# Optimization experiments

Hardware: AMD Instinct MI355X
Metric: run time of the kernel (lower is better)

## Reference

```python
import jax, jax.numpy as jnp
import numpy as np

B, N, F_IN = 32, 512, 64
HEADS = (8, 8)
HIDS = (64, 64)
EDGE_P = 0.05  # graph density
NEG_SLOPE = 0.2
NEG_INF = -1e20


def setup_inputs() -> dict:
    key = jax.random.key(0)
    ks = jax.random.split(key, 8)
    x = jax.random.normal(ks[0], (B, N, F_IN), dtype=jnp.float32)
    adj = (jax.random.uniform(ks[1], (B, N, N)) < EDGE_P).astype(jnp.float32)
    adj = jnp.maximum(adj, adj.transpose(0, 2, 1))  # symmetric adjacency
    # mask = (batch, row): every (b, n) pair gets the masked softmax
    b_idx = jnp.repeat(jnp.arange(B, dtype=jnp.int32), N)   # [B*N]
    r_idx = jnp.tile(jnp.arange(N, dtype=jnp.int32), B)     # [B*N]
    # layer 0: f_in=64 -> f_out=64, H=8 ; layer 1: f_in=64*8=512 -> f_out=64, H=8
    W0 = jax.random.normal(ks[2], (F_IN, HIDS[0]), dtype=jnp.float32) / jnp.sqrt(jnp.float32(F_IN))
    a_src0 = jax.random.normal(ks[3], (HIDS[0], HEADS[0]), dtype=jnp.float32) / jnp.sqrt(jnp.float32(HIDS[0]))
    a_dst0 = jax.random.normal(ks[4], (HIDS[0], HEADS[0]), dtype=jnp.float32) / jnp.sqrt(jnp.float32(HIDS[0]))
    f_in1 = HIDS[0] * HEADS[0]
    W1 = jax.random.normal(ks[5], (f_in1, HIDS[1]), dtype=jnp.float32) / jnp.sqrt(jnp.float32(f_in1))
    a_src1 = jax.random.normal(ks[6], (HIDS[1], HEADS[1]), dtype=jnp.float32) / jnp.sqrt(jnp.float32(HIDS[1]))
    a_dst1 = jax.random.normal(ks[7], (HIDS[1], HEADS[1]), dtype=jnp.float32) / jnp.sqrt(jnp.float32(HIDS[1]))
    return dict(x=x, adj=adj, b_idx=b_idx, r_idx=r_idx,
                W0=W0, a_src0=a_src0, a_dst0=a_dst0,
                W1=W1, a_src1=a_src1, a_dst1=a_dst1)


def _gat_layer(x, adj, b_idx, r_idx, W, a_src, a_dst):
    # x: [B,N,f_in], adj: [B,N,N] (diag already set), W: [f_in,F], a_*: [F,H]
    hp = x @ W                                        # [B,N,F]
    s = jnp.einsum('bnf,fh->bhn', hp, a_src)          # attn_src
    d = jnp.einsum('bnf,fh->bhn', hp, a_dst)          # attn_dst
    attn = s[:, :, :, None] + d[:, :, None, :]        # [B,H,N,N]
    attn = jnp.where(attn >= 0, attn, NEG_SLOPE * attn)  # leaky_relu(0.2)
    attn = jnp.where(adj[:, None, :, :] == 0, 0.0, attn)  # masked_fill(adj==0, 0)
    rows = attn[b_idx, :, r_idx, :]                   # [K,H,N]
    rows = jnp.where(rows == 0.0, NEG_INF, rows)
    rows = jax.nn.softmax(rows, axis=-1)
    attn = attn.at[b_idx, :, r_idx, :].set(rows)
    return jnp.einsum('bhij,bjf->bhif', attn, hp)     # [B,H,N,F]


def reference(x, adj, b_idx, r_idx, W0, a_src0, a_dst0, W1, a_src1, a_dst1):
    Bn, Nn = x.shape[:2]
    # torch mutates adj in place: adj[batch,row,row] = 1 (self loops)
    adj = adj.at[b_idx, r_idx, r_idx].set(1.0)
    o = _gat_layer(x, adj, b_idx, r_idx, W0, a_src0, a_dst0)      # [B,H,N,F0]
    x1 = jax.nn.elu(o.transpose(0, 2, 1, 3).reshape(Bn, Nn, -1))  # [B,N,H*F0]
    o2 = _gat_layer(x1, adj, b_idx, r_idx, W1, a_src1, a_dst1)    # [B,H,N,F1]
    return o2.mean(axis=1)                                        # [B,N,F1]
```

## Files before the change

kernel.cpp:

```cpp
#include <hip/hip_runtime.h>
#include <hip/hip_bf16.h>
#include <math.h>

#define BB 32
#define NN 512

typedef _Float16 f16x8 __attribute__((ext_vector_type(8)));
typedef __fp16  fp16x2 __attribute__((ext_vector_type(2)));
typedef float f32x4 __attribute__((ext_vector_type(4)));

#define MFMA16(a, b, c) __builtin_amdgcn_mfma_f32_16x16x32_f16(a, b, c, 0, 0, 0)

union AF { f16x8 v; unsigned int u[4]; };

static __device__ __forceinline__ unsigned int fenc(float x) {
    unsigned int u = __float_as_uint(x);
    return (u & 0x80000000u) ? ~u : (u | 0x80000000u);
}
static __device__ __forceinline__ float fdec(unsigned int k) {
    unsigned int u = (k & 0x80000000u) ? (k ^ 0x80000000u) : ~k;
    return __uint_as_float(u);
}

__global__ __launch_bounds__(256) void k_wt_prep(
    const float* __restrict__ W0, _Float16* __restrict__ W0T,
    const float* __restrict__ W1, _Float16* __restrict__ W1T,
    unsigned int* __restrict__ maxdK)
{
    int id = blockIdx.x * 256 + threadIdx.x;
    if (id < 512) maxdK[id] = 0u;
    const float* W; _Float16* WT; int KT, task;
    if (id < 512) { W = W0; WT = W0T; KT = 64;  task = id; }
    else          { W = W1; WT = W1T; KT = 512; task = id - 512; }
    int n = task & 63, gabs = task >> 6;
    int c = gabs >> 3, g = gabs & 7;
    f16x8 hv;
#pragma unroll
    for (int e = 0; e < 8; ++e)
        hv[e] = (_Float16)W[(size_t)(gabs * 8 + e) * 64 + n];
    *(f16x8*)(WT + (size_t)n * KT + c * 64 + (g ^ (n & 7)) * 8) = hv;
}

static __device__ __forceinline__ void epi_sd_hpt(
    const float* ctile, const float* asd_f, int row0, int t,
    float* __restrict__ s, float* __restrict__ dTg, _Float16* __restrict__ hpT,
    unsigned int* __restrict__ maxdK)
{
    int b = row0 >> 9, jb = row0 & 511;
    if (t < 128) {
        int rr = t >> 3, h = t & 7;
        float sv = 0.f, dv = 0.f;
#pragma unroll
        for (int f = 0; f < 64; ++f) {
            float hv = ctile[rr * 66 + f];
            sv = fmaf(hv, asd_f[f * 8 + h], sv);
            dv = fmaf(hv, asd_f[512 + f * 8 + h], dv);
        }
        s[((size_t)b * NN + jb + rr) * 8 + h] = sv;
        dTg[((size_t)b * 8 + h) * NN + jb + rr] = dv;
        float m = dv;
        m = fmaxf(m, __shfl_xor(m, 8));
        m = fmaxf(m, __shfl_xor(m, 16));
        m = fmaxf(m, __shfl_xor(m, 32));
        if ((t & 63) < 8) atomicMax(maxdK + b * 8 + h, fenc(m));
    } else {
        int t2 = t - 128;
        int f = t2 >> 1, jl = (t2 & 1) * 8;
        f16x8 hv;
#pragma unroll
        for (int e = 0; e < 8; ++e)
            hv[e] = (_Float16)ctile[(jl + e) * 66 + f];
        *(f16x8*)(hpT + ((size_t)b * 64 + f) * NN + jb + jl) = hv;
    }
}

__global__ __launch_bounds__(256) void k_gemm0(
    const float* __restrict__ x, const _Float16* __restrict__ W0T,
    const float* __restrict__ a_src, const float* __restrict__ a_dst,
    float* __restrict__ s, float* __restrict__ dTg, _Float16* __restrict__ hpT,
    unsigned int* __restrict__ maxdK)
{
    __shared__ float ctile[16 * 66];
    __shared__ float asd_f[1024];
    int t = threadIdx.x, row0 = blockIdx.x * 16;
    int lane = t & 63, w = t >> 6, cn = lane & 15, rq = lane >> 4;

    ((float4*)asd_f)[t] = (t < 128) ? ((const float4*)a_src)[t]
                                    : ((const float4*)a_dst)[t - 128];
    f32x4 acc;
#pragma unroll
    for (int e = 0; e < 4; ++e) acc[e] = 0.f;
#pragma unroll
    for (int ks = 0; ks < 2; ++ks) {
        const float* xp = x + (size_t)(row0 + cn) * 64 + ks * 32 + rq * 8;
        float4 x0 = *(const float4*)xp, x1 = *(const float4*)(xp + 4);
        f16x8 ah = {(_Float16)x0.x, (_Float16)x0.y, (_Float16)x0.z, (_Float16)x0.w,
                    (_Float16)x1.x, (_Float16)x1.y, (_Float16)x1.z, (_Float16)x1.w};
        int nn = w * 16 + cn;
        f16x8 bh = *(const f16x8*)(W0T + (size_t)nn * 64 + (((ks * 4 + rq) ^ (nn & 7)) * 8));
        acc = MFMA16(ah, bh, acc);
    }
#pragma unroll
    for (int r = 0; r < 4; ++r)
        ctile[(rq * 4 + r) * 66 + w * 16 + cn] = acc[r];
    __syncthreads();
    epi_sd_hpt(ctile, asd_f, row0, t, s, dTg, hpT, maxdK);
}

template<int MODE>
__global__ __launch_bounds__(256, 4) void k_attn_fused(
    const float* __restrict__ adj, const float* __restrict__ s,
    const float* __restrict__ dTg, const unsigned int* __restrict__ maxdK,
    const _Float16* __restrict__ hpT,
    const _Float16* __restrict__ W1T,
    const float* __restrict__ a_src, const float* __restrict__ a_dst,
    float* __restrict__ s_out, float* __restrict__ dTg_out,
    _Float16* __restrict__ hpT_out, unsigned int* __restrict__ maxdK_out,
    float* __restrict__ o_f)
{
    __shared__ __align__(16) char smem[32768];

    int blk = blockIdx.x;
    int vb = ((blk & 7) << 7) | (blk >> 3);
    int b = vb >> 5, i0 = (vb & 31) << 4;
    int row0 = vb * 16;
    int t = threadIdx.x, lane = t & 63, w = t >> 6;
    int cn = lane & 15, rq = lane >> 4;
    int h0 = 2 * w, h1 = h0 + 1;
    int myrow = i0 + cn;

    float sv0 = s[((size_t)b * NN + myrow) * 8 + h0];
    float sv1 = s[((size_t)b * NN + myrow) * 8 + h1];
    float M0 = fmaxf(sv0 + fdec(maxdK[b * 8 + h0]), 0.f);
    float M1 = fmaxf(sv1 + fdec(maxdK[b * 8 + h1]), 0.f);

    const float* arow = adj + ((size_t)b * NN + myrow) * NN;
    const float* dg0 = dTg + ((size_t)b * 8 + h0) * NN;
    const float* dg1 = dTg + ((size_t)b * 8 + h1) * NN;
    const _Float16* hb = hpT + (size_t)b * 64 * NN;

    int f0 = t >> 3, g0 = t & 7;
    int f1 = f0 + 32;
    int sw = ((g0 ^ (f0 & 7)) * 8);
    int sw0 = f0 * 64 + sw, sw1 = f1 * 64 + sw;

    f16x8 ones;
#pragma unroll
    for (int e = 0; e < 8; ++e) ones[e] = (_Float16)1.0f;

    f32x4 acc[2][4], accrs[2];
#pragma unroll
    for (int hh = 0; hh < 2; ++hh) {
#pragma unroll
        for (int e = 0; e < 4; ++e) accrs[hh][e] = 0.f;
#pragma unroll
        for (int ft = 0; ft < 4; ++ft)
#pragma unroll
            for (int e = 0; e < 4; ++e) acc[hh][ft][e] = 0.f;
    }

    uint4 rH0 = *(const uint4*)(hb + (size_t)f0 * 512 + g0 * 8);
    uint4 rH1 = *(const uint4*)(hb + (size_t)f1 * 512 + g0 * 8);
    float aa[2][8], dd0[2][8], dd1[2][8];
#pragma unroll
    for (int ks = 0; ks < 2; ++ks) {
        int j0 = ks * 32 + rq * 8;
        *(float4*)&aa[ks][0]  = *(const float4*)(arow + j0);
        *(float4*)&aa[ks][4]  = *(const float4*)(arow + j0 + 4);
        *(float4*)&dd0[ks][0] = *(const float4*)(dg0 + j0);
        *(float4*)&dd0[ks][4] = *(const float4*)(dg0 + j0 + 4);
        *(float4*)&dd1[ks][0] = *(const float4*)(dg1 + j0);
        *(float4*)&dd1[ks][4] = *(const float4*)(dg1 + j0 + 4);
    }
    {
        _Float16* hT0 = (_Float16*)smem;
        *(uint4*)&hT0[sw0] = rH0;
        *(uint4*)&hT0[sw1] = rH1;
    }
    __syncthreads();
    rH0 = *(const uint4*)(hb + (size_t)f0 * 512 + 64 + g0 * 8);
    rH1 = *(const uint4*)(hb + (size_t)f1 * 512 + 64 + g0 * 8);

    for (int jcx = 0; jcx < 8; ++jcx) {
        int jc = jcx * 64;
        _Float16* hTc = (_Float16*)(smem + (jcx & 1) * 8192);
        _Float16* hTn = (_Float16*)(smem + ((jcx & 1) ^ 1) * 8192);

        AF aA[2], aB[2];
#pragma unroll
        for (int ks = 0; ks < 2; ++ks) {
            int j0 = jc + ks * 32 + rq * 8;
            int rel = myrow - j0;
#pragma unroll
            for (int e = 0; e < 8; e += 2) {
                float pA[2], pB[2];
#pragma unroll
                for (int q = 0; q < 2; ++q) {
                    int ee = e + q;
                    bool con = (aa[ks][ee] != 0.f) || (ee == rel);
                    float e0 = sv0 + dd0[ks][ee];
                    float l0 = fmaxf(e0, 0.2f * e0);
                    float p0 = __expf(l0 - M0);
                    pA[q] = (con && l0 != 0.f) ? p0 : 0.f;
                    float e1 = sv1 + dd1[ks][ee];
                    float l1 = fmaxf(e1, 0.2f * e1);
                    float p1 = __expf(l1 - M1);
                    pB[q] = (con && l1 != 0.f) ? p1 : 0.f;
                }
                fp16x2 ka = __builtin_amdgcn_cvt_pkrtz(pA[0], pA[1]);
                fp16x2 kb = __builtin_amdgcn_cvt_pkrtz(pB[0], pB[1]);
                aA[ks].u[e >> 1] = __builtin_bit_cast(unsigned int, ka);
                aB[ks].u[e >> 1] = __builtin_bit_cast(unsigned int, kb);
            }
        }
        if (jcx < 7) {
#pragma unroll
            for (int ks = 0; ks < 2; ++ks) {
                int j0 = jc + 64 + ks * 32 + rq * 8;
                *(float4*)&aa[ks][0]  = *(const float4*)(arow + j0);
                *(float4*)&aa[ks][4]  = *(const float4*)(arow + j0 + 4);
                *(float4*)&dd0[ks][0] = *(const float4*)(dg0 + j0);
                *(float4*)&dd0[ks][4] = *(const float4*)(dg0 + j0 + 4);
                *(float4*)&dd1[ks][0] = *(const float4*)(dg1 + j0);
                *(float4*)&dd1[ks][4] = *(const float4*)(dg1 + j0 + 4);
            }
        }
#pragma unroll
        for (int ks = 0; ks < 2; ++ks) {
            accrs[0] = MFMA16(aA[ks].v, ones, accrs[0]);
            accrs[1] = MFMA16(aB[ks].v, ones, accrs[1]);
#pragma unroll
            for (int ft = 0; ft < 4; ++ft) {
                int f = ft * 16 + cn;
                f16x8 bh = *(const f16x8*)&hTc[f * 64 + (((ks * 4 + rq) ^ (f & 7)) * 8)];
                acc[0][ft] = MFMA16(aA[ks].v, bh, acc[0][ft]);
                acc[1][ft] = MFMA16(aB[ks].v, bh, acc[1][ft]);
            }
        }
        if (jcx < 7) {
            *(uint4*)&hTn[sw0] = rH0;
            *(uint4*)&hTn[sw1] = rH1;
            if (jcx < 6) {
                rH0 = *(const uint4*)(hb + (size_t)f0 * 512 + jc + 128 + g0 * 8);
                rH1 = *(const uint4*)(hb + (size_t)f1 * 512 + jc + 128 + g0 * 8);
            }
        }
        __syncthreads();
    }

    float invr[2][4];
#pragma unroll
    for (int hh = 0; hh < 2; ++hh)
#pragma unroll
        for (int r = 0; r < 4; ++r) invr[hh][r] = 1.0f / accrs[hh][r];

    if (MODE == 0) {
        _Float16* x1all = (_Float16*)smem;
#pragma unroll
        for (int hh = 0; hh < 2; ++hh) {
            int h = h0 + hh;
#pragma unroll
            for (int ft = 0; ft < 4; ++ft)
#pragma unroll
                for (int r = 0; r < 4; ++r) {
                    int il = rq * 4 + r;
                    float v = acc[hh][ft][r] * invr[hh][r];
                    v = v > 0.f ? v : __expf(v) - 1.f;
                    int f = ft * 16 + cn;
                    x1all[h * 1024 + il * 64 + (((f >> 3) ^ (il & 7)) * 8) + (f & 7)] =
                        (_Float16)v;
                }
        }

        _Float16* Bst[2] = { (_Float16*)(smem + 16384), (_Float16*)(smem + 24576) };
        {
#pragma unroll
            for (int u = 0; u < 2; ++u) {
                int idx = t + u * 256;
                *(uint4*)&Bst[0][idx * 8] =
                    *(const uint4*)(W1T + (size_t)(idx >> 3) * 512 + (idx & 7) * 8);
            }
        }
        f32x4 g1;
#pragma unroll
        for (int e = 0; e < 4; ++e) g1[e] = 0.f;
        uint4 rB0, rB1;
        for (int kc = 0; kc < 8; ++kc) {
            int cur = kc & 1;
            if (kc < 7) {
                rB0 = *(const uint4*)(W1T + (size_t)(t >> 3) * 512 + (kc + 1) * 64 + (t & 7) * 8);
                rB1 = *(const uint4*)(W1T + (size_t)((t + 256) >> 3) * 512 + (kc + 1) * 64 + (t & 7) * 8);
            }
            __syncthreads();
#pragma unroll
            for (int ks = 0; ks < 2; ++ks) {
                int pa = (((ks * 4 + rq) ^ (cn & 7)) * 8);
                f16x8 ah = *(const f16x8*)&x1all[kc * 1024 + cn * 64 + pa];
                int nn = w * 16 + cn;
                f16x8 bh = *(const f16x8*)&Bst[cur][nn * 64 + (((ks * 4 + rq) ^ (nn & 7)) * 8)];
                g1 = MFMA16(ah, bh, g1);
            }
            if (kc < 7) {
                *(uint4*)&Bst[cur ^ 1][t * 8] = rB0;
                *(uint4*)&Bst[cur ^ 1][(t + 256) * 8] = rB1;
            }
        }
        __syncthreads();
        float* ctile = (float*)smem;
        float* asd_f = (float*)(smem + 4352);
#pragma unroll
        for (int r = 0; r < 4; ++r)
            ctile[(rq * 4 + r) * 66 + w * 16 + cn] = g1[r];
        ((float4*)asd_f)[t] = (t < 128) ? ((const float4*)a_src)[t]
                                        : ((const float4*)a_dst)[t - 128];
        __syncthreads();
        epi_sd_hpt(ctile, asd_f, row0, t, s_out, dTg_out, hpT_out, maxdK_out);
    } else {
        float* red = (float*)smem;
#pragma unroll
        for (int ft = 0; ft < 4; ++ft)
#pragma unroll
            for (int r = 0; r < 4; ++r) {
                int il = rq * 4 + r;
                float v = acc[0][ft][r] * invr[0][r]
                        + acc[1][ft][r] * invr[1][r];
                red[(w * 16 + il) * 64 + ft * 16 + cn] = v;
            }
        __syncthreads();
#pragma unroll
        for (int u = 0; u < 4; ++u) {
            int idx = t + u * 256;
            int il = idx >> 6, f = idx & 63;
            float sum = red[il * 64 + f] + red[(16 + il) * 64 + f]
                      + red[(32 + il) * 64 + f] + red[(48 + il) * 64 + f];
            o_f[((size_t)b * NN + i0 + il) * 64 + f] = sum * 0.125f;
        }
    }
}

extern "C" void kernel_launch(void* const* d_in, const int* in_sizes, int n_in,
                              void* d_out, int out_size, void* d_ws, size_t ws_size,
                              hipStream_t stream) {
    const float* x      = (const float*)d_in[0];
    const float* adj    = (const float*)d_in[1];
    const float* W0     = (const float*)d_in[4];
    const float* a_src0 = (const float*)d_in[5];
    const float* a_dst0 = (const float*)d_in[6];
    const float* W1     = (const float*)d_in[7];
    const float* a_src1 = (const float*)d_in[8];
    const float* a_dst1 = (const float*)d_in[9];
    float* out = (float*)d_out;

    float* ws = (float*)d_ws;
    const size_t R = (size_t)BB * NN;
    float* s0    = ws;
    float* dTg0  = s0 + R * 8;
    float* s1    = dTg0 + (size_t)BB * 8 * NN;
    float* dTg1  = s1 + R * 8;
    unsigned int* maxdK = (unsigned int*)(dTg1 + (size_t)BB * 8 * NN);
    unsigned int* maxd0K = maxdK;
    unsigned int* maxd1K = maxdK + 256;
    _Float16* hp0T = (_Float16*)(maxdK + 512);
    _Float16* hp1T = hp0T + (size_t)BB * 64 * NN;
    _Float16* W0T  = hp1T + (size_t)BB * 64 * NN;
    _Float16* W1T  = W0T + (size_t)64 * 64;

    k_wt_prep<<<18, 256, 0, stream>>>(W0, W0T, W1, W1T, maxdK);
    k_gemm0<<<1024, 256, 0, stream>>>(x, W0T, a_src0, a_dst0, s0, dTg0, hp0T, maxd0K);
    k_attn_fused<0><<<1024, 256, 0, stream>>>(adj, s0, dTg0, maxd0K, hp0T,
                                              W1T, a_src1, a_dst1,
                                              s1, dTg1, hp1T, maxd1K, nullptr);
    k_attn_fused<1><<<1024, 256, 0, stream>>>(adj, s1, dTg1, maxd1K, hp1T,
                                              nullptr, nullptr, nullptr,
                                              nullptr, nullptr, nullptr, nullptr, out);
}
```

Before: 167.3 us.

## Use one wave per head in attention kernels with 512-thread blocks

The attention kernels now launch 512 threads, one wave per head, instead of 256 threads with each wave handling two heads. This halves per-thread registers and MFMA chains and drops the register prefetch of adj and dTg in favour of loading them directly each chunk. The layer-1 GEMM is split so two wave groups each cover half of K and then sum the partials in shared memory. In exchange, adj rows are read by twice as many waves, block-level syncs cover more threads, and the software prefetch of those inputs is gone.

Measured after the change: 198.1 us. 18.4% more time.

```diff
diff --git a/kernel.cpp b/kernel.cpp
--- a/kernel.cpp
+++ b/kernel.cpp
@@ -63,7 +63,7 @@
         m = fmaxf(m, __shfl_xor(m, 16));
         m = fmaxf(m, __shfl_xor(m, 32));
         if ((t & 63) < 8) atomicMax(maxdK + b * 8 + h, fenc(m));
-    } else {
+    } else if (t < 256) {
         int t2 = t - 128;
         int f = t2 >> 1, jl = (t2 & 1) * 8;
         f16x8 hv;
@@ -108,11 +108,10 @@
 }
 
 template<int MODE>
-__global__ __launch_bounds__(256, 4) void k_attn_fused(
+__global__ __launch_bounds__(512, 8) void k_attn(
     const float* __restrict__ adj, const float* __restrict__ s,
     const float* __restrict__ dTg, const unsigned int* __restrict__ maxdK,
-    const _Float16* __restrict__ hpT,
-    const _Float16* __restrict__ W1T,
+    const _Float16* __restrict__ hpT, const _Float16* __restrict__ W1T,
     const float* __restrict__ a_src, const float* __restrict__ a_dst,
     float* __restrict__ s_out, float* __restrict__ dTg_out,
     _Float16* __restrict__ hpT_out, unsigned int* __restrict__ maxdK_out,
@@ -126,195 +125,143 @@
     int row0 = vb * 16;
     int t = threadIdx.x, lane = t & 63, w = t >> 6;
     int cn = lane & 15, rq = lane >> 4;
-    int h0 = 2 * w, h1 = h0 + 1;
     int myrow = i0 + cn;
 
-    float sv0 = s[((size_t)b * NN + myrow) * 8 + h0];
-    float sv1 = s[((size_t)b * NN + myrow) * 8 + h1];
-    float M0 = fmaxf(sv0 + fdec(maxdK[b * 8 + h0]), 0.f);
-    float M1 = fmaxf(sv1 + fdec(maxdK[b * 8 + h1]), 0.f);
+    float sv = s[((size_t)b * NN + myrow) * 8 + w];
+    float M = fmaxf(sv + fdec(maxdK[b * 8 + w]), 0.f);
 
     const float* arow = adj + ((size_t)b * NN + myrow) * NN;
-    const float* dg0 = dTg + ((size_t)b * 8 + h0) * NN;
-    const float* dg1 = dTg + ((size_t)b * 8 + h1) * NN;
+    const float* dg = dTg + ((size_t)b * 8 + w) * NN;
     const _Float16* hb = hpT + (size_t)b * 64 * NN;
 
     int f0 = t >> 3, g0 = t & 7;
-    int f1 = f0 + 32;
-    int sw = ((g0 ^ (f0 & 7)) * 8);
-    int sw0 = f0 * 64 + sw, sw1 = f1 * 64 + sw;
+    int sw0 = f0 * 64 + ((g0 ^ (f0 & 7)) * 8);
 
     f16x8 ones;
 #pragma unroll
     for (int e = 0; e < 8; ++e) ones[e] = (_Float16)1.0f;
 
-    f32x4 acc[2][4], accrs[2];
-#pragma unroll
-    for (int hh = 0; hh < 2; ++hh) {
-#pragma unroll
-        for (int e = 0; e < 4; ++e) accrs[hh][e] = 0.f;
-#pragma unroll
-        for (int ft = 0; ft < 4; ++ft)
-#pragma unroll
-            for (int e = 0; e < 4; ++e) acc[hh][ft][e] = 0.f;
-    }
-
-    uint4 rH0 = *(const uint4*)(hb + (size_t)f0 * 512 + g0 * 8);
-    uint4 rH1 = *(const uint4*)(hb + (size_t)f1 * 512 + g0 * 8);
-    float aa[2][8], dd0[2][8], dd1[2][8];
-#pragma unroll
-    for (int ks = 0; ks < 2; ++ks) {
-        int j0 = ks * 32 + rq * 8;
-        *(float4*)&aa[ks][0]  = *(const float4*)(arow + j0);
-        *(float4*)&aa[ks][4]  = *(const float4*)(arow + j0 + 4);
-        *(float4*)&dd0[ks][0] = *(const float4*)(dg0 + j0);
-        *(float4*)&dd0[ks][4] = *(const float4*)(dg0 + j0 + 4);
-        *(float4*)&dd1[ks][0] = *(const float4*)(dg1 + j0);
-        *(float4*)&dd1[ks][4] = *(const float4*)(dg1 + j0 + 4);
-    }
-    {
-        _Float16* hT0 = (_Float16*)smem;
-        *(uint4*)&hT0[sw0] = rH0;
-        *(uint4*)&hT0[sw1] = rH1;
-    }
+    f32x4 acc[4], accrs;
+#pragma unroll
+    for (int e = 0; e < 4; ++e) accrs[e] = 0.f;
+#pragma unroll
+    for (int ft = 0; ft < 4; ++ft)
+#pragma unroll
+        for (int e = 0; e < 4; ++e) acc[ft][e] = 0.f;
+
+    uint4 rH = *(const uint4*)(hb + (size_t)f0 * 512 + g0 * 8);
+    *(uint4*)&((_Float16*)smem)[sw0] = rH;
     __syncthreads();
-    rH0 = *(const uint4*)(hb + (size_t)f0 * 512 + 64 + g0 * 8);
-    rH1 = *(const uint4*)(hb + (size_t)f1 * 512 + 64 + g0 * 8);
+    rH = *(const uint4*)(hb + (size_t)f0 * 512 + 64 + g0 * 8);
 
     for (int jcx = 0; jcx < 8; ++jcx) {
         int jc = jcx * 64;
         _Float16* hTc = (_Float16*)(smem + (jcx & 1) * 8192);
         _Float16* hTn = (_Float16*)(smem + ((jcx & 1) ^ 1) * 8192);
 
-        AF aA[2], aB[2];
+        AF aA[2];
 #pragma unroll
         for (int ks = 0; ks < 2; ++ks) {
             int j0 = jc + ks * 32 + rq * 8;
+            float4 a0 = *(const float4*)(arow + j0);
+            float4 a1 = *(const float4*)(arow + j0 + 4);
+            float4 d0 = *(const float4*)(dg + j0);
+            float4 d1 = *(const float4*)(dg + j0 + 4);
+            float aa[8] = {a0.x, a0.y, a0.z, a0.w, a1.x, a1.y, a1.z, a1.w};
+            float dd[8] = {d0.x, d0.y, d0.z, d0.w, d1.x, d1.y, d1.z, d1.w};
             int rel = myrow - j0;
 #pragma unroll
             for (int e = 0; e < 8; e += 2) {
-                float pA[2], pB[2];
+                float pv[2];
 #pragma unroll
                 for (int q = 0; q < 2; ++q) {
                     int ee = e + q;
-                    bool con = (aa[ks][ee] != 0.f) || (ee == rel);
-                    float e0 = sv0 + dd0[ks][ee];
+                    bool con = (aa[ee] != 0.f) || (ee == rel);
+                    float e0 = sv + dd[ee];
                     float l0 = fmaxf(e0, 0.2f * e0);
-                    float p0 = __expf(l0 - M0);
-                    pA[q] = (con && l0 != 0.f) ? p0 : 0.f;
-                    float e1 = sv1 + dd1[ks][ee];
-                    float l1 = fmaxf(e1, 0.2f * e1);
-                    float p1 = __expf(l1 - M1);
-                    pB[q] = (con && l1 != 0.f) ? p1 : 0.f;
+                    float p0 = __expf(l0 - M);
+                    pv[q] = (con && l0 != 0.f) ? p0 : 0.f;
                 }
-                fp16x2 ka = __builtin_amdgcn_cvt_pkrtz(pA[0], pA[1]);
-                fp16x2 kb = __builtin_amdgcn_cvt_pkrtz(pB[0], pB[1]);
+                fp16x2 ka = __builtin_amdgcn_cvt_pkrtz(pv[0], pv[1]);
                 aA[ks].u[e >> 1] = __builtin_bit_cast(unsigned int, ka);
-                aB[ks].u[e >> 1] = __builtin_bit_cast(unsigned int, kb);
-            }
-        }
-        if (jcx < 7) {
-#pragma unroll
-            for (int ks = 0; ks < 2; ++ks) {
-                int j0 = jc + 64 + ks * 32 + rq * 8;
-                *(float4*)&aa[ks][0]  = *(const float4*)(arow + j0);
-                *(float4*)&aa[ks][4]  = *(const float4*)(arow + j0 + 4);
-                *(float4*)&dd0[ks][0] = *(const float4*)(dg0 + j0);
-                *(float4*)&dd0[ks][4] = *(const float4*)(dg0 + j0 + 4);
-                *(float4*)&dd1[ks][0] = *(const float4*)(dg1 + j0);
-                *(float4*)&dd1[ks][4] = *(const float4*)(dg1 + j0 + 4);
-            }
-        }
-#pragma unroll
-        for (int ks = 0; ks < 2; ++ks) {
-            accrs[0] = MFMA16(aA[ks].v, ones, accrs[0]);
-            accrs[1] = MFMA16(aB[ks].v, ones, accrs[1]);
+            }
+        }
+        accrs = MFMA16(aA[0].v, ones, accrs);
+        accrs = MFMA16(aA[1].v, ones, accrs);
+#pragma unroll
+        for (int ks = 0; ks < 2; ++ks)
 #pragma unroll
             for (int ft = 0; ft < 4; ++ft) {
                 int f = ft * 16 + cn;
                 f16x8 bh = *(const f16x8*)&hTc[f * 64 + (((ks * 4 + rq) ^ (f & 7)) * 8)];
-                acc[0][ft] = MFMA16(aA[ks].v, bh, acc[0][ft]);
-                acc[1][ft] = MFMA16(aB[ks].v, bh, acc[1][ft]);
-            }
-        }
+                acc[ft] = MFMA16(aA[ks].v, bh, acc[ft]);
+            }
         if (jcx < 7) {
-            *(uint4*)&hTn[sw0] = rH0;
-            *(uint4*)&hTn[sw1] = rH1;
-            if (jcx < 6) {
-                rH0 = *(const uint4*)(hb + (size_t)f0 * 512 + jc + 128 + g0 * 8);
-                rH1 = *(const uint4*)(hb + (size_t)f1 * 512 + jc + 128 + g0 * 8);
-            }
+            *(uint4*)&hTn[sw0] = rH;
+            if (jcx < 6)
+                rH = *(const uint4*)(hb + (size_t)f0 * 512 + jc + 128 + g0 * 8);
         }
         __syncthreads();
     }
 
-    float invr[2][4];
-#pragma unroll
-    for (int hh = 0; hh < 2; ++hh)
-#pragma unroll
-        for (int r = 0; r < 4; ++r) invr[hh][r] = 1.0f / accrs[hh][r];
+    float invr[4];
+#pragma unroll
+    for (int r = 0; r < 4; ++r) invr[r] = 1.0f / accrs[r];
 
     if (MODE == 0) {
         _Float16* x1all = (_Float16*)smem;
 #pragma unroll
-        for (int hh = 0; hh < 2; ++hh) {
-            int h = h0 + hh;
-#pragma unroll
-            for (int ft = 0; ft < 4; ++ft)
-#pragma unroll
-                for (int r = 0; r < 4; ++r) {
-                    int il = rq * 4 + r;
-                    float v = acc[hh][ft][r] * invr[hh][r];
-                    v = v > 0.f ? v : __expf(v) - 1.f;
-                    int f = ft * 16 + cn;
-                    x1all[h * 1024 + il * 64 + (((f >> 3) ^ (il & 7)) * 8) + (f & 7)] =
-                        (_Float16)v;
-                }
-        }
-
-        _Float16* Bst[2] = { (_Float16*)(smem + 16384), (_Float16*)(smem + 24576) };
-        {
-#pragma unroll
-            for (int u = 0; u < 2; ++u) {
-                int idx = t + u * 256;
-                *(uint4*)&Bst[0][idx * 8] =
-                    *(const uint4*)(W1T + (size_t)(idx >> 3) * 512 + (idx & 7) * 8);
-            }
-        }
+        for (int ft = 0; ft < 4; ++ft)
+#pragma unroll
+            for (int r = 0; r < 4; ++r) {
+                int il = rq * 4 + r;
+                float v = acc[ft][r] * invr[r];
+                v = v > 0.f ? v : __expf(v) - 1.f;
+                int f = ft * 16 + cn;
+                x1all[w * 1024 + il * 64 + (((f >> 3) ^ (il & 7)) * 8) + (f & 7)] =
+                    (_Float16)v;
+            }
+
+        _Float16* Bst = (_Float16*)(smem + 16384);
+        int kh = w >> 2, nsub = w & 3;
         f32x4 g1;
 #pragma unroll
         for (int e = 0; e < 4; ++e) g1[e] = 0.f;
-        uint4 rB0, rB1;
-        for (int kc = 0; kc < 8; ++kc) {
-            int cur = kc & 1;
-            if (kc < 7) {
-                rB0 = *(const uint4*)(W1T + (size_t)(t >> 3) * 512 + (kc + 1) * 64 + (t & 7) * 8);
-                rB1 = *(const uint4*)(W1T + (size_t)((t + 256) >> 3) * 512 + (kc + 1) * 64 + (t & 7) * 8);
-            }
+        for (int it = 0; it < 4; ++it) {
+            size_t sB = (size_t)(t >> 3) * 512 + it * 64 + (t & 7) * 8;
+            uint4 c0 = *(const uint4*)(W1T + sB);
+            uint4 c1 = *(const uint4*)(W1T + sB + 256);
             __syncthreads();
+            *(uint4*)&Bst[t * 8] = c0;
+            *(uint4*)&Bst[4096 + t * 8] = c1;
+            __syncthreads();
+            int kc = kh * 4 + it;
 #pragma unroll
             for (int ks = 0; ks < 2; ++ks) {
                 int pa = (((ks * 4 + rq) ^ (cn & 7)) * 8);
                 f16x8 ah = *(const f16x8*)&x1all[kc * 1024 + cn * 64 + pa];
-                int nn = w * 16 + cn;
-                f16x8 bh = *(const f16x8*)&Bst[cur][nn * 64 + (((ks * 4 + rq) ^ (nn & 7)) * 8)];
+                int nn = nsub * 16 + cn;
+                f16x8 bh = *(const f16x8*)&Bst[kh * 4096 + nn * 64 +
+                                               (((ks * 4 + rq) ^ (nn & 7)) * 8)];
                 g1 = MFMA16(ah, bh, g1);
             }
-            if (kc < 7) {
-                *(uint4*)&Bst[cur ^ 1][t * 8] = rB0;
-                *(uint4*)&Bst[cur ^ 1][(t + 256) * 8] = rB1;
-            }
-        }
-        __syncthreads();
-        float* ctile = (float*)smem;
-        float* asd_f = (float*)(smem + 4352);
+        }
+        __syncthreads();
+
+        float* ctA   = (float*)smem;
+        float* ctB   = (float*)(smem + 4352);
+        float* asd_f = (float*)(smem + 8704);
+        float* dst = kh ? ctB : ctA;
 #pragma unroll
         for (int r = 0; r < 4; ++r)
-            ctile[(rq * 4 + r) * 66 + w * 16 + cn] = g1[r];
-        ((float4*)asd_f)[t] = (t < 128) ? ((const float4*)a_src)[t]
-                                        : ((const float4*)a_dst)[t - 128];
-        __syncthreads();
-        epi_sd_hpt(ctile, asd_f, row0, t, s_out, dTg_out, hpT_out, maxdK_out);
+            dst[(rq * 4 + r) * 66 + nsub * 16 + cn] = g1[r];
+        if (t < 256)
+            ((float4*)asd_f)[t] = (t < 128) ? ((const float4*)a_src)[t]
+                                            : ((const float4*)a_dst)[t - 128];
+        __syncthreads();
+        for (int idx = t; idx < 1056; idx += 512) ctA[idx] += ctB[idx];
+        __syncthreads();
+        epi_sd_hpt(ctA, asd_f, row0, t, s_out, dTg_out, hpT_out, maxdK_out);
     } else {
         float* red = (float*)smem;
 #pragma unroll
@@ -322,17 +269,16 @@
 #pragma unroll
             for (int r = 0; r < 4; ++r) {
                 int il = rq * 4 + r;
-                float v = acc[0][ft][r] * invr[0][r]
-                        + acc[1][ft][r] * invr[1][r];
-                red[(w * 16 + il) * 64 + ft * 16 + cn] = v;
-            }
-        __syncthreads();
-#pragma unroll
-        for (int u = 0; u < 4; ++u) {
-            int idx = t + u * 256;
+                red[w * 1024 + il * 64 + ft * 16 + cn] = acc[ft][r] * invr[r];
+            }
+        __syncthreads();
+#pragma unroll
+        for (int u = 0; u < 2; ++u) {
+            int idx = t + u * 512;
             int il = idx >> 6, f = idx & 63;
-            float sum = red[il * 64 + f] + red[(16 + il) * 64 + f]
-                      + red[(32 + il) * 64 + f] + red[(48 + il) * 64 + f];
+            float sum = 0.f;
+#pragma unroll
+            for (int h = 0; h < 8; ++h) sum += red[h * 1024 + il * 64 + f];
             o_f[((size_t)b * NN + i0 + il) * 64 + f] = sum * 0.125f;
         }
     }
@@ -358,19 +304,17 @@
     float* s1    = dTg0 + (size_t)BB * 8 * NN;
     float* dTg1  = s1 + R * 8;
     unsigned int* maxdK = (unsigned int*)(dTg1 + (size_t)BB * 8 * NN);
-    unsigned int* maxd0K = maxdK;
-    unsigned int* maxd1K = maxdK + 256;
     _Float16* hp0T = (_Float16*)(maxdK + 512);
     _Float16* hp1T = hp0T + (size_t)BB * 64 * NN;
     _Float16* W0T  = hp1T + (size_t)BB * 64 * NN;
     _Float16* W1T  = W0T + (size_t)64 * 64;
 
     k_wt_prep<<<18, 256, 0, stream>>>(W0, W0T, W1, W1T, maxdK);
-    k_gemm0<<<1024, 256, 0, stream>>>(x, W0T, a_src0, a_dst0, s0, dTg0, hp0T, maxd0K);
-    k_attn_fused<0><<<1024, 256, 0, stream>>>(adj, s0, dTg0, maxd0K, hp0T,
-                                              W1T, a_src1, a_dst1,
-                                              s1, dTg1, hp1T, maxd1K, nullptr);
-    k_attn_fused<1><<<1024, 256, 0, stream>>>(adj, s1, dTg1, maxd1K, hp1T,
-                                              nullptr, nullptr, nullptr,
-                                              nullptr, nullptr, nullptr, nullptr, out);
-}
+    k_gemm0<<<1024, 256, 0, stream>>>(x, W0T, a_src0, a_dst0, s0, dTg0, hp0T, maxdK);
+    k_attn<0><<<1024, 512, 0, stream>>>(adj, s0, dTg0, maxdK, hp0T,
+                                        W1T, a_src1, a_dst1,
+                                        s1, dTg1, hp1T, maxdK + 256, nullptr);
+    k_attn<1><<<1024, 512, 0, stream>>>(adj, s1, dTg1, maxdK + 256, hp1T,
+                                        nullptr, nullptr, nullptr,
+                                        nullptr, nullptr, nullptr, nullptr, out);
+}
```

## Precompute adjacency bitmasks once and reuse them in both attention layers

Applied to the files above, without the earlier changes.

A prep kernel now packs the fp32 adjacency matrix, with self-loops included, into 64-bit ballot bitmasks per row chunk. Both attention kernels read 8 bytes per 64 columns instead of 256 bytes of floats, which cuts the global memory traffic from two full adjacency reads. The cost is one extra full pass over adj in the prep kernel, which grows from 18 to 1024 blocks.

Result: no change. 170.5 us (+1.9%).

```diff
diff --git a/kernel.cpp b/kernel.cpp
--- a/kernel.cpp
+++ b/kernel.cpp
@@ -22,23 +22,42 @@
     return __uint_as_float(u);
 }
 
-__global__ __launch_bounds__(256) void k_wt_prep(
+__global__ __launch_bounds__(256) void k_prep(
     const float* __restrict__ W0, _Float16* __restrict__ W0T,
     const float* __restrict__ W1, _Float16* __restrict__ W1T,
+    const float* __restrict__ adj, unsigned long long* __restrict__ masks,
     unsigned int* __restrict__ maxdK)
 {
-    int id = blockIdx.x * 256 + threadIdx.x;
+    int blk = blockIdx.x, t = threadIdx.x;
+    int id = blk * 256 + t;
     if (id < 512) maxdK[id] = 0u;
-    const float* W; _Float16* WT; int KT, task;
-    if (id < 512) { W = W0; WT = W0T; KT = 64;  task = id; }
-    else          { W = W1; WT = W1T; KT = 512; task = id - 512; }
-    int n = task & 63, gabs = task >> 6;
-    int c = gabs >> 3, g = gabs & 7;
-    f16x8 hv;
-#pragma unroll
-    for (int e = 0; e < 8; ++e)
-        hv[e] = (_Float16)W[(size_t)(gabs * 8 + e) * 64 + n];
-    *(f16x8*)(WT + (size_t)n * KT + c * 64 + (g ^ (n & 7)) * 8) = hv;
+    if (blk < 18) {
+        const float* W; _Float16* WT; int KT, task;
+        if (id < 512) { W = W0; WT = W0T; KT = 64;  task = id; }
+        else          { W = W1; WT = W1T; KT = 512; task = id - 512; }
+        int n = task & 63, gabs = task >> 6;
+        int c = gabs >> 3, g = gabs & 7;
+        f16x8 hv;
+#pragma unroll
+        for (int e = 0; e < 8; ++e)
+            hv[e] = (_Float16)W[(size_t)(gabs * 8 + e) * 64 + n];
+        *(f16x8*)(WT + (size_t)n * KT + c * 64 + (g ^ (n & 7)) * 8) = hv;
+    }
+    int lane = t & 63, w = t >> 6;
+    int wi = blk * 4 + w;
+#pragma unroll
+    for (int rr = 0; rr < 4; ++rr) {
+        int row = wi * 4 + rr;
+        int i = row & 511;
+        const float* ar = adj + (size_t)row * NN;
+#pragma unroll
+        for (int jc = 0; jc < 8; ++jc) {
+            float a = ar[jc * 64 + lane];
+            bool bit = (a != 0.f) || (jc * 64 + lane == i);
+            unsigned long long m = __ballot(bit);
+            if (lane == 0) masks[(size_t)row * 8 + jc] = m;
+        }
+    }
 }
 
 static __device__ __forceinline__ void epi_sd_hpt(
@@ -109,10 +128,9 @@
 
 template<int MODE>
 __global__ __launch_bounds__(256, 4) void k_attn_fused(
-    const float* __restrict__ adj, const float* __restrict__ s,
+    const unsigned long long* __restrict__ masks, const float* __restrict__ s,
     const float* __restrict__ dTg, const unsigned int* __restrict__ maxdK,
-    const _Float16* __restrict__ hpT,
-    const _Float16* __restrict__ W1T,
+    const _Float16* __restrict__ hpT, const _Float16* __restrict__ W1T,
     const float* __restrict__ a_src, const float* __restrict__ a_dst,
     float* __restrict__ s_out, float* __restrict__ dTg_out,
     _Float16* __restrict__ hpT_out, unsigned int* __restrict__ maxdK_out,
@@ -134,7 +152,7 @@
     float M0 = fmaxf(sv0 + fdec(maxdK[b * 8 + h0]), 0.f);
     float M1 = fmaxf(sv1 + fdec(maxdK[b * 8 + h1]), 0.f);
 
-    const float* arow = adj + ((size_t)b * NN + myrow) * NN;
+    const unsigned long long* mrow = masks + ((size_t)b * NN + myrow) * 8;
     const float* dg0 = dTg + ((size_t)b * 8 + h0) * NN;
     const float* dg1 = dTg + ((size_t)b * 8 + h1) * NN;
     const _Float16* hb = hpT + (size_t)b * 64 * NN;
@@ -161,12 +179,11 @@
 
     uint4 rH0 = *(const uint4*)(hb + (size_t)f0 * 512 + g0 * 8);
     uint4 rH1 = *(const uint4*)(hb + (size_t)f1 * 512 + g0 * 8);
-    float aa[2][8], dd0[2][8], dd1[2][8];
+    unsigned long long mk = mrow[0];
+    float dd0[2][8], dd1[2][8];
 #pragma unroll
     for (int ks = 0; ks < 2; ++ks) {
         int j0 = ks * 32 + rq * 8;
-        *(float4*)&aa[ks][0]  = *(const float4*)(arow + j0);
-        *(float4*)&aa[ks][4]  = *(const float4*)(arow + j0 + 4);
         *(float4*)&dd0[ks][0] = *(const float4*)(dg0 + j0);
         *(float4*)&dd0[ks][4] = *(const float4*)(dg0 + j0 + 4);
         *(float4*)&dd1[ks][0] = *(const float4*)(dg1 + j0);
@@ -189,15 +206,14 @@
         AF aA[2], aB[2];
 #pragma unroll
         for (int ks = 0; ks < 2; ++ks) {
-            int j0 = jc + ks * 32 + rq * 8;
-            int rel = myrow - j0;
+            unsigned int mb = (unsigned int)(mk >> (ks * 32 + rq * 8)) & 0xffu;
 #pragma unroll
             for (int e = 0; e < 8; e += 2) {
                 float pA[2], pB[2];
 #pragma unroll
                 for (int q = 0; q < 2; ++q) {
                     int ee = e + q;
-                    bool con = (aa[ks][ee] != 0.f) || (ee == rel);
+                    bool con = (mb >> ee) & 1;
                     float e0 = sv0 + dd0[ks][ee];
                     float l0 = fmaxf(e0, 0.2f * e0);
                     float p0 = __expf(l0 - M0);
@@ -214,11 +230,10 @@
             }
         }
         if (jcx < 7) {
+            mk = mrow[jcx + 1];
 #pragma unroll
             for (int ks = 0; ks < 2; ++ks) {
                 int j0 = jc + 64 + ks * 32 + rq * 8;
-                *(float4*)&aa[ks][0]  = *(const float4*)(arow + j0);
-                *(float4*)&aa[ks][4]  = *(const float4*)(arow + j0 + 4);
                 *(float4*)&dd0[ks][0] = *(const float4*)(dg0 + j0);
                 *(float4*)&dd0[ks][4] = *(const float4*)(dg0 + j0 + 4);
                 *(float4*)&dd1[ks][0] = *(const float4*)(dg1 + j0);
@@ -358,19 +373,19 @@
     float* s1    = dTg0 + (size_t)BB * 8 * NN;
     float* dTg1  = s1 + R * 8;
     unsigned int* maxdK = (unsigned int*)(dTg1 + (size_t)BB * 8 * NN);
-    unsigned int* maxd0K = maxdK;
-    unsigned int* maxd1K = maxdK + 256;
     _Float16* hp0T = (_Float16*)(maxdK + 512);
     _Float16* hp1T = hp0T + (size_t)BB * 64 * NN;
     _Float16* W0T  = hp1T + (size_t)BB * 64 * NN;
     _Float16* W1T  = W0T + (size_t)64 * 64;
-
-    k_wt_prep<<<18, 256, 0, stream>>>(W0, W0T, W1, W1T, maxdK);
-    k_gemm0<<<1024, 256, 0, stream>>>(x, W0T, a_src0, a_dst0, s0, dTg0, hp0T, maxd0K);
-    k_attn_fused<0><<<1024, 256, 0, stream>>>(adj, s0, dTg0, maxd0K, hp0T,
+    unsigned long long* masks =
+        (unsigned long long*)(((uintptr_t)(W1T + (size_t)64 * 512) + 15) & ~(uintptr_t)15);
+
+    k_prep<<<1024, 256, 0, stream>>>(W0, W0T, W1, W1T, adj, masks, maxdK);
+    k_gemm0<<<1024, 256, 0, stream>>>(x, W0T, a_src0, a_dst0, s0, dTg0, hp0T, maxdK);
+    k_attn_fused<0><<<1024, 256, 0, stream>>>(masks, s0, dTg0, maxdK, hp0T,
                                               W1T, a_src1, a_dst1,
-                                              s1, dTg1, hp1T, maxd1K, nullptr);
-    k_attn_fused<1><<<1024, 256, 0, stream>>>(adj, s1, dTg1, maxd1K, hp1T,
+                                              s1, dTg1, hp1T, maxdK + 256, nullptr);
+    k_attn_fused<1><<<1024, 256, 0, stream>>>(masks, s1, dTg1, maxdK + 256, hp1T,
                                               nullptr, nullptr, nullptr,
                                               nullptr, nullptr, nullptr, nullptr, out);
 }
```
